# Kernel optimization log

Measured on AMD Instinct MI355X. Metric: run time of the kernel, lower is better.

Reference implementation:

```python
import jax, jax.numpy as jnp
import numpy as np

D_MODEL, D_K, D_V, H = 512, 64, 64, 8
B, NQ, NK = 2, 4096, 4096


def setup_inputs() -> dict:
    key = jax.random.key(0)
    ks = jax.random.split(key, 11)
    def xavier(k, shape):
        fan_in, fan_out = shape[1], shape[0]
        lim = jnp.sqrt(6.0 / (fan_in + fan_out))
        return jax.random.uniform(k, shape, jnp.float32, -lim, lim)
    return {
        "queries": jax.random.normal(ks[0], (B, NQ, D_MODEL), jnp.float32),
        "keys": jax.random.normal(ks[1], (B, NK, D_MODEL), jnp.float32),
        "values": jax.random.normal(ks[2], (B, NK, D_MODEL), jnp.float32),
        "Wq": xavier(ks[3], (H * D_K, D_MODEL)),
        "bq": jnp.zeros((H * D_K,), jnp.float32),
        "Wk": xavier(ks[4], (H * D_K, D_MODEL)),
        "bk": jnp.zeros((H * D_K,), jnp.float32),
        "Wv": xavier(ks[5], (H * D_V, D_MODEL)),
        "bv": jnp.zeros((H * D_V,), jnp.float32),
        "Wo": xavier(ks[6], (D_MODEL, H * D_V)),
        "bo": jnp.zeros((D_MODEL,), jnp.float32),
    }


def reference(queries, keys, values, Wq, bq, Wk, bk, Wv, bv, Wo, bo):
    b_s, nq, _ = queries.shape
    nk = keys.shape[1]
    # QKV projections (torch Linear: x @ W.T + b)
    q = (queries @ Wq.T + bq).reshape(b_s, nq, H, D_K).transpose(0, 2, 1, 3)  # b h nq dk
    k = (keys @ Wk.T + bk).reshape(b_s, nk, H, D_K).transpose(0, 2, 1, 3)     # b h nk dk
    v = (values @ Wv.T + bv).reshape(b_s, nk, H, D_V).transpose(0, 2, 1, 3)   # b h nk dv
    att = jnp.einsum("bhqd,bhkd->bhqk", q, k) / jnp.sqrt(jnp.float32(D_K))
    att = jax.nn.softmax(att, axis=-1)
    # dropout is identity in eval mode
    out = jnp.einsum("bhqk,bhkd->bhqd", att, v)
    out = out.transpose(0, 2, 1, 3).reshape(b_s, nq, H * D_V)
    return out @ Wo.T + bo
```

## Files before the change

### kernel.cpp

```cpp
#include <hip/hip_runtime.h>
#include <hip/hip_bf16.h>


typedef __attribute__((ext_vector_type(8))) short bf16x8;
typedef __attribute__((ext_vector_type(4))) float f32x4;
typedef __attribute__((ext_vector_type(16))) float f32x16;
typedef __attribute__((ext_vector_type(2))) int int2v;

#define SEQ  4096
#define DM   512
#define FPAD 72
#define VPAD 136
#define QSCALE 0.18033688011112042f
#define FSHIFT 16.0f

__device__ inline float fast_exp2(float x) {
#if __has_builtin(__builtin_amdgcn_exp2f)
    return __builtin_amdgcn_exp2f(x);
#else
    return __expf(x * 0.69314718056f);
#endif
}

__device__ inline unsigned pk2(float x, float y) {
#if __has_builtin(__builtin_amdgcn_cvt_pk_bf16_f32)
    typedef __attribute__((ext_vector_type(2))) __bf16 bf16x2_t;
    bf16x2_t h = __builtin_amdgcn_cvt_pk_bf16_f32(x, y);
    return *(unsigned*)&h;
#else
    unsigned ux = __float_as_uint(x);
    unsigned uy = __float_as_uint(y);
    ux += 0x7fff + ((ux >> 16) & 1);
    uy += 0x7fff + ((uy >> 16) & 1);
    return (ux >> 16) | (uy & 0xffff0000u);
#endif
}

__device__ inline int2v swap_half(unsigned a, unsigned b, int h) {
#if __has_builtin(__builtin_amdgcn_permlane32_swap)
    (void)h;
    return __builtin_amdgcn_permlane32_swap((int)a, (int)b, false, false);
#else
    unsigned ax = (unsigned)__shfl_xor((int)a, 32);
    unsigned bx = (unsigned)__shfl_xor((int)b, 32);
    int2v r;
    r.x = h ? (int)bx : (int)a;
    r.y = h ? (int)b  : (int)ax;
    return r;
#endif
}

__global__ __launch_bounds__(256) void cvt_w(
    const float* __restrict__ w0, const float* __restrict__ w1,
    const float* __restrict__ w2, const float* __restrict__ w3,
    __hip_bfloat16* __restrict__ o0, __hip_bfloat16* __restrict__ o1,
    __hip_bfloat16* __restrict__ o2, __hip_bfloat16* __restrict__ o3)
{
    const float* w = (blockIdx.y == 0) ? w0 : (blockIdx.y == 1) ? w1
                   : (blockIdx.y == 2) ? w2 : w3;
    __hip_bfloat16* o = (blockIdx.y == 0) ? o0 : (blockIdx.y == 1) ? o1
                      : (blockIdx.y == 2) ? o2 : o3;
    const int i = (blockIdx.x * 256 + threadIdx.x) * 4;
    float4 v = *(const float4*)&w[i];
    uint2 p;
    p.x = pk2(v.x, v.y);
    p.y = pk2(v.z, v.w);
    *(uint2*)&((unsigned short*)o)[i] = p;
}

__global__ __launch_bounds__(256) void qkv_proj(
    const float* __restrict__ Xq, const float* __restrict__ Xk, const float* __restrict__ Xv,
    const __hip_bfloat16* __restrict__ Wq16, const __hip_bfloat16* __restrict__ Wk16,
    const __hip_bfloat16* __restrict__ Wv16,
    const float* __restrict__ bq, const float* __restrict__ bk, const float* __restrict__ bv,
    __hip_bfloat16* __restrict__ Oq, __hip_bfloat16* __restrict__ Ok,
    __hip_bfloat16* __restrict__ Ovt)
{
    const int z = blockIdx.z;
    const float* A          = (z == 0) ? Xq : (z == 1) ? Xk : Xv;
    const __hip_bfloat16* W = (z == 0) ? Wq16 : (z == 1) ? Wk16 : Wv16;
    const float* bias       = (z == 0) ? bq : (z == 1) ? bk : bv;

    __shared__ __align__(16) short As[64 * 32];
    __shared__ __align__(16) short Ws2[128 * 32];

    const int bm   = blockIdx.x * 64;
    const int bn   = blockIdx.y * 128;
    const int tid  = threadIdx.x;
    const int wave = tid >> 6;
    const int lane = tid & 63;
    const int quad = lane >> 4;
    const int l16  = lane & 15;

    const int srow = tid >> 2;
    const int scol = (tid & 3) * 8;

    f32x4 acc[8] = {};

    float4 a0 = *(const float4*)&A[(size_t)(bm + srow) * DM + scol];
    float4 a1 = *(const float4*)&A[(size_t)(bm + srow) * DM + scol + 4];
    bf16x8 w0 = *(const bf16x8*)&W[(size_t)(bn + srow) * DM + scol];
    bf16x8 w1 = *(const bf16x8*)&W[(size_t)(bn + srow + 64) * DM + scol];

    for (int k0 = 0; k0 < DM; k0 += 32) {
        uint4 pa = {pk2(a0.x, a0.y), pk2(a0.z, a0.w), pk2(a1.x, a1.y), pk2(a1.z, a1.w)};

        __syncthreads();
        *(uint4*)&As[srow * 32 + scol] = pa;
        *(bf16x8*)&Ws2[srow * 32 + scol] = w0;
        *(bf16x8*)&Ws2[(srow + 64) * 32 + scol] = w1;
        __syncthreads();

        if (k0 + 32 < DM) {
            a0 = *(const float4*)&A[(size_t)(bm + srow) * DM + k0 + 32 + scol];
            a1 = *(const float4*)&A[(size_t)(bm + srow) * DM + k0 + 32 + scol + 4];
            w0 = *(const bf16x8*)&W[(size_t)(bn + srow) * DM + k0 + 32 + scol];
            w1 = *(const bf16x8*)&W[(size_t)(bn + srow + 64) * DM + k0 + 32 + scol];
        }

        bf16x8 a = *(bf16x8*)&As[(wave * 16 + l16) * 32 + quad * 8];
#pragma unroll
        for (int nt = 0; nt < 8; nt++) {
            bf16x8 b = *(bf16x8*)&Ws2[(nt * 16 + l16) * 32 + quad * 8];
            acc[nt] = __builtin_amdgcn_mfma_f32_16x16x32_bf16(a, b, acc[nt], 0, 0, 0);
        }
    }

    if (z == 2) {
        const int row0 = bm + wave * 16 + quad * 4;
        const int b    = row0 >> 12;
        const int seq0 = row0 & 4095;
        unsigned short* Vt = (unsigned short*)Ovt;
#pragma unroll
        for (int nt = 0; nt < 8; nt++) {
            const int col = bn + nt * 16 + l16;
            const float bv_ = bias[col];
            uint2 pk;
            pk.x = pk2(acc[nt][0] + bv_, acc[nt][1] + bv_);
            pk.y = pk2(acc[nt][2] + bv_, acc[nt][3] + bv_);
            *(uint2*)&Vt[((size_t)(b * 512 + col)) * 4096 + seq0] = pk;
        }
    } else {
        unsigned short* C = (unsigned short*)((z == 0) ? Oq : Ok);
        const float scale = (z == 0) ? QSCALE : 1.0f;
        const size_t row0 = bm + wave * 16 + quad * 4;
#pragma unroll
        for (int nt = 0; nt < 8; nt++) {
            const int col = bn + nt * 16 + l16;
            const float bv_ = bias[col];
            unsigned u01 = pk2((acc[nt][0] + bv_) * scale, (acc[nt][1] + bv_) * scale);
            unsigned u23 = pk2((acc[nt][2] + bv_) * scale, (acc[nt][3] + bv_) * scale);
            C[(row0 + 0) * DM + col] = (unsigned short)(u01 & 0xffff);
            C[(row0 + 1) * DM + col] = (unsigned short)(u01 >> 16);
            C[(row0 + 2) * DM + col] = (unsigned short)(u23 & 0xffff);
            C[(row0 + 3) * DM + col] = (unsigned short)(u23 >> 16);
        }
    }
}

__global__ __launch_bounds__(256, 4) void flash_attn(
    const __hip_bfloat16* __restrict__ Q,
    const __hip_bfloat16* __restrict__ K,
    const __hip_bfloat16* __restrict__ Vt,
    __hip_bfloat16* __restrict__ O)
{
    __shared__ __align__(16) short Ks[128 * FPAD];
    __shared__ __align__(16) short Vs[64 * VPAD];

    const int q0  = blockIdx.x * 128;
    const int bh  = blockIdx.y;
    const int tid = threadIdx.x;
    const int wave = tid >> 6;
    const int lane = tid & 63;
    const int L = lane & 31;
    const int h = lane >> 5;

    const __hip_bfloat16* Qb = Q + (size_t)(bh >> 3) * SEQ * DM + (bh & 7) * 64;
    const __hip_bfloat16* Kb = K + (size_t)(bh >> 3) * SEQ * DM + (bh & 7) * 64;
    const __hip_bfloat16* Vb = Vt + (size_t)bh * 64 * SEQ;
    __hip_bfloat16*       Ob = O + (size_t)(bh >> 3) * SEQ * DM + (bh & 7) * 64;

    const int kr = tid >> 3;
    const int kc = (tid & 7) * 8;
    const int vr = tid >> 4;
    const int vc = (tid & 15) * 8;

    const int qrow = q0 + wave * 32 + L;
    bf16x8 bq[4];
#pragma unroll
    for (int db = 0; db < 4; db++)
        bq[db] = *(const bf16x8*)&Qb[(size_t)qrow * DM + db * 16 + h * 8];

    const __hip_bfloat16* kg = Kb + (size_t)kr * DM + kc;
    const __hip_bfloat16* vg = Vb + (size_t)vr * SEQ + vc;

    bf16x8 kp[4], vp[4];
#pragma unroll
    for (int i = 0; i < 4; i++) {
        kp[i] = *(const bf16x8*)(kg + (size_t)i * 32 * DM);
        vp[i] = *(const bf16x8*)(vg + (size_t)i * 16 * SEQ);
    }

    const short* ksb = &Ks[L * FPAD + h * 8];
    const short* vsb = &Vs[L * VPAD + h * 8];

    f32x16 oacc[2] = {};
    float lsum = 0.0f;

    for (int kv0 = 0; kv0 < SEQ; kv0 += 128) {
        __syncthreads();
#pragma unroll
        for (int i = 0; i < 4; i++) {
            *(bf16x8*)&Ks[(kr + i * 32) * FPAD + kc] = kp[i];
            *(bf16x8*)&Vs[(vr + i * 16) * VPAD + vc] = vp[i];
        }
        __syncthreads();

        kg += (size_t)128 * DM;
        vg += 128;
        if (kv0 + 128 < SEQ) {
#pragma unroll
            for (int i = 0; i < 4; i++) {
                kp[i] = *(const bf16x8*)(kg + (size_t)i * 32 * DM);
                vp[i] = *(const bf16x8*)(vg + (size_t)i * 16 * SEQ);
            }
        }

#pragma unroll
        for (int kb = 0; kb < 4; kb++) {
            f32x16 s = {};
            __builtin_amdgcn_s_setprio(1);
#pragma unroll
            for (int db = 0; db < 4; db++) {
                bf16x8 ak = *(const bf16x8*)&ksb[(kb * 32) * FPAD + db * 16];
                s = __builtin_amdgcn_mfma_f32_32x32x16_bf16(ak, bq[db], s, 0, 0, 0);
            }
            __builtin_amdgcn_s_setprio(0);

#pragma unroll
            for (int r = 0; r < 16; r++) s[r] = fast_exp2(s[r] - FSHIFT);

            unsigned pk_[8];
#pragma unroll
            for (int j = 0; j < 8; j++) pk_[j] = pk2(s[2 * j], s[2 * j + 1]);

#pragma unroll
            for (int j = 0; j < 8; j++)
                lsum += __uint_as_float(pk_[j] << 16)
                      + __uint_as_float(pk_[j] & 0xffff0000u);

            int2v w0 = swap_half(pk_[0], pk_[2], h);
            int2v w1 = swap_half(pk_[1], pk_[3], h);
            int2v w2 = swap_half(pk_[4], pk_[6], h);
            int2v w3 = swap_half(pk_[5], pk_[7], h);
            uint4 f0u = {(unsigned)w0.x, (unsigned)w1.x, (unsigned)w0.y, (unsigned)w1.y};
            uint4 f1u = {(unsigned)w2.x, (unsigned)w3.x, (unsigned)w2.y, (unsigned)w3.y};
            bf16x8 fg0 = *(bf16x8*)&f0u;
            bf16x8 fg1 = *(bf16x8*)&f1u;

            __builtin_amdgcn_s_setprio(1);
#pragma unroll
            for (int dvb = 0; dvb < 2; dvb++) {
                bf16x8 av0 = *(const bf16x8*)&vsb[(dvb * 32) * VPAD + kb * 32];
                bf16x8 av1 = *(const bf16x8*)&vsb[(dvb * 32) * VPAD + kb * 32 + 16];
                oacc[dvb] = __builtin_amdgcn_mfma_f32_32x32x16_bf16(av0, fg0, oacc[dvb], 0, 0, 0);
                oacc[dvb] = __builtin_amdgcn_mfma_f32_32x32x16_bf16(av1, fg1, oacc[dvb], 0, 0, 0);
            }
            __builtin_amdgcn_s_setprio(0);
        }
    }

    const float tot = lsum + __shfl_xor(lsum, 32);
    const float inv = 1.0f / tot;

    unsigned short* Op = (unsigned short*)Ob;
#pragma unroll
    for (int dvb = 0; dvb < 2; dvb++)
#pragma unroll
        for (int b = 0; b < 4; b++) {
            uint2 ov;
            ov.x = pk2(oacc[dvb][4 * b + 0] * inv, oacc[dvb][4 * b + 1] * inv);
            ov.y = pk2(oacc[dvb][4 * b + 2] * inv, oacc[dvb][4 * b + 3] * inv);
            *(uint2*)&Op[(size_t)qrow * DM + dvb * 32 + b * 8 + h * 4] = ov;
        }
}

__global__ __launch_bounds__(256) void out_proj(
    const __hip_bfloat16* __restrict__ A,
    const __hip_bfloat16* __restrict__ W,
    const float* __restrict__ bias,
    float* __restrict__ C)
{
    __shared__ __align__(16) short As[64 * 32];
    __shared__ __align__(16) short Ws2[128 * 32];

    const int bm   = blockIdx.x * 64;
    const int bn   = blockIdx.y * 128;
    const int tid  = threadIdx.x;
    const int wave = tid >> 6;
    const int lane = tid & 63;
    const int quad = lane >> 4;
    const int l16  = lane & 15;

    const int srow = tid >> 2;
    const int scol = (tid & 3) * 8;

    f32x4 acc[8] = {};

    bf16x8 ap = *(const bf16x8*)&A[(size_t)(bm + srow) * DM + scol];
    bf16x8 w0 = *(const bf16x8*)&W[(size_t)(bn + srow) * DM + scol];
    bf16x8 w1 = *(const bf16x8*)&W[(size_t)(bn + srow + 64) * DM + scol];

    for (int k0 = 0; k0 < DM; k0 += 32) {
        __syncthreads();
        *(bf16x8*)&As[srow * 32 + scol] = ap;
        *(bf16x8*)&Ws2[srow * 32 + scol] = w0;
        *(bf16x8*)&Ws2[(srow + 64) * 32 + scol] = w1;
        __syncthreads();

        if (k0 + 32 < DM) {
            ap = *(const bf16x8*)&A[(size_t)(bm + srow) * DM + k0 + 32 + scol];
            w0 = *(const bf16x8*)&W[(size_t)(bn + srow) * DM + k0 + 32 + scol];
            w1 = *(const bf16x8*)&W[(size_t)(bn + srow + 64) * DM + k0 + 32 + scol];
        }

        bf16x8 a = *(bf16x8*)&As[(wave * 16 + l16) * 32 + quad * 8];
#pragma unroll
        for (int nt = 0; nt < 8; nt++) {
            bf16x8 b = *(bf16x8*)&Ws2[(nt * 16 + l16) * 32 + quad * 8];
            acc[nt] = __builtin_amdgcn_mfma_f32_16x16x32_bf16(a, b, acc[nt], 0, 0, 0);
        }
    }

#pragma unroll
    for (int nt = 0; nt < 8; nt++) {
        const int col = bn + nt * 16 + l16;
        const float bv_ = bias[col];
#pragma unroll
        for (int r = 0; r < 4; r++) {
            const int row = bm + wave * 16 + quad * 4 + r;
            C[(size_t)row * DM + col] = acc[nt][r] + bv_;
        }
    }
}

extern "C" void kernel_launch(void* const* d_in, const int* in_sizes, int n_in,
                              void* d_out, int out_size, void* d_ws, size_t ws_size,
                              hipStream_t stream) {
    const float* queries = (const float*)d_in[0];
    const float* keys    = (const float*)d_in[1];
    const float* values  = (const float*)d_in[2];
    const float* Wq = (const float*)d_in[3];
    const float* bq = (const float*)d_in[4];
    const float* Wk = (const float*)d_in[5];
    const float* bk = (const float*)d_in[6];
    const float* Wv = (const float*)d_in[7];
    const float* bv = (const float*)d_in[8];
    const float* Wo = (const float*)d_in[9];
    const float* bo = (const float*)d_in[10];
    float* out = (float*)d_out;

    const size_t MS = (size_t)2 * SEQ * DM;
    const size_t WN = (size_t)DM * DM;
    __hip_bfloat16* q_ws  = (__hip_bfloat16*)d_ws;
    __hip_bfloat16* k_ws  = q_ws + MS;
    __hip_bfloat16* vt_ws = k_ws + MS;
    __hip_bfloat16* o_ws  = vt_ws + MS;
    __hip_bfloat16* wq16  = o_ws + MS;
    __hip_bfloat16* wk16  = wq16 + WN;
    __hip_bfloat16* wv16  = wk16 + WN;
    __hip_bfloat16* wo16  = wv16 + WN;

    dim3 blk(256);

    cvt_w<<<dim3(256, 4), blk, 0, stream>>>(Wq, Wk, Wv, Wo, wq16, wk16, wv16, wo16);

    qkv_proj<<<dim3(128, 4, 3), blk, 0, stream>>>(
        queries, keys, values, wq16, wk16, wv16, bq, bk, bv, q_ws, k_ws, vt_ws);

    flash_attn<<<dim3(32, 16), blk, 0, stream>>>(q_ws, k_ws, vt_ws, o_ws);

    out_proj<<<dim3(128, 4), blk, 0, stream>>>(o_ws, wo16, bo, out);
}
```

Before: 251.3 us.

## Split KV tiles across two wave groups in flash attention with LDS reduction

Doubles the flash attention block to 512 threads: four query-row groups times two KV groups, each KV group handling half of every 128-key tile. This gives more waves per query tile to hide latency and halves per-thread global loads. Partial outputs and row sums are combined through shared memory at the end. The softmax shift is folded into the MFMA accumulator init, and the row sum is taken from fp32 values instead of the bf16-rounded ones. The costs are an extra reduction, more register and LDS pressure per block, and possibly lower occupancy under the 512-thread launch bound.

```diff
diff --git a/kernel.cpp b/kernel.cpp
--- a/kernel.cpp
+++ b/kernel.cpp
@@ -158,7 +158,7 @@
     }
 }
 
-__global__ __launch_bounds__(256, 4) void flash_attn(
+__global__ __launch_bounds__(512, 4) void flash_attn(
     const __hip_bfloat16* __restrict__ Q,
     const __hip_bfloat16* __restrict__ K,
     const __hip_bfloat16* __restrict__ Vt,
@@ -174,6 +174,8 @@
     const int lane = tid & 63;
     const int L = lane & 31;
     const int h = lane >> 5;
+    const int qg  = wave & 3;
+    const int kvg = wave >> 2;
 
     const __hip_bfloat16* Qb = Q + (size_t)(bh >> 3) * SEQ * DM + (bh & 7) * 64;
     const __hip_bfloat16* Kb = K + (size_t)(bh >> 3) * SEQ * DM + (bh & 7) * 64;
@@ -185,7 +187,7 @@
     const int vr = tid >> 4;
     const int vc = (tid & 15) * 8;
 
-    const int qrow = q0 + wave * 32 + L;
+    const int qrow = q0 + qg * 32 + L;
     bf16x8 bq[4];
 #pragma unroll
     for (int db = 0; db < 4; db++)
@@ -194,41 +196,41 @@
     const __hip_bfloat16* kg = Kb + (size_t)kr * DM + kc;
     const __hip_bfloat16* vg = Vb + (size_t)vr * SEQ + vc;
 
-    bf16x8 kp[4], vp[4];
-#pragma unroll
-    for (int i = 0; i < 4; i++) {
-        kp[i] = *(const bf16x8*)(kg + (size_t)i * 32 * DM);
-        vp[i] = *(const bf16x8*)(vg + (size_t)i * 16 * SEQ);
-    }
+    bf16x8 kp[2], vp[2];
+    kp[0] = *(const bf16x8*)(kg);
+    kp[1] = *(const bf16x8*)(kg + (size_t)64 * DM);
+    vp[0] = *(const bf16x8*)(vg);
+    vp[1] = *(const bf16x8*)(vg + (size_t)32 * SEQ);
 
     const short* ksb = &Ks[L * FPAD + h * 8];
     const short* vsb = &Vs[L * VPAD + h * 8];
 
     f32x16 oacc[2] = {};
-    float lsum = 0.0f;
+    float l0 = 0.0f, l1 = 0.0f;
 
     for (int kv0 = 0; kv0 < SEQ; kv0 += 128) {
         __syncthreads();
-#pragma unroll
-        for (int i = 0; i < 4; i++) {
-            *(bf16x8*)&Ks[(kr + i * 32) * FPAD + kc] = kp[i];
-            *(bf16x8*)&Vs[(vr + i * 16) * VPAD + vc] = vp[i];
-        }
+        *(bf16x8*)&Ks[kr * FPAD + kc] = kp[0];
+        *(bf16x8*)&Ks[(kr + 64) * FPAD + kc] = kp[1];
+        *(bf16x8*)&Vs[vr * VPAD + vc] = vp[0];
+        *(bf16x8*)&Vs[(vr + 32) * VPAD + vc] = vp[1];
         __syncthreads();
 
         kg += (size_t)128 * DM;
         vg += 128;
         if (kv0 + 128 < SEQ) {
-#pragma unroll
-            for (int i = 0; i < 4; i++) {
-                kp[i] = *(const bf16x8*)(kg + (size_t)i * 32 * DM);
-                vp[i] = *(const bf16x8*)(vg + (size_t)i * 16 * SEQ);
-            }
-        }
-
-#pragma unroll
-        for (int kb = 0; kb < 4; kb++) {
-            f32x16 s = {};
+            kp[0] = *(const bf16x8*)(kg);
+            kp[1] = *(const bf16x8*)(kg + (size_t)64 * DM);
+            vp[0] = *(const bf16x8*)(vg);
+            vp[1] = *(const bf16x8*)(vg + (size_t)32 * SEQ);
+        }
+
+#pragma unroll
+        for (int kb2 = 0; kb2 < 2; kb2++) {
+            const int kb = kvg * 2 + kb2;
+            f32x16 s;
+#pragma unroll
+            for (int r = 0; r < 16; r++) s[r] = -FSHIFT;
             __builtin_amdgcn_s_setprio(1);
 #pragma unroll
             for (int db = 0; db < 4; db++) {
@@ -238,16 +240,14 @@
             __builtin_amdgcn_s_setprio(0);
 
 #pragma unroll
-            for (int r = 0; r < 16; r++) s[r] = fast_exp2(s[r] - FSHIFT);
+            for (int r = 0; r < 16; r++) s[r] = fast_exp2(s[r]);
+
+#pragma unroll
+            for (int r = 0; r < 16; r += 2) { l0 += s[r]; l1 += s[r + 1]; }
 
             unsigned pk_[8];
 #pragma unroll
             for (int j = 0; j < 8; j++) pk_[j] = pk2(s[2 * j], s[2 * j + 1]);
-
-#pragma unroll
-            for (int j = 0; j < 8; j++)
-                lsum += __uint_as_float(pk_[j] << 16)
-                      + __uint_as_float(pk_[j] & 0xffff0000u);
 
             int2v w0 = swap_half(pk_[0], pk_[2], h);
             int2v w1 = swap_half(pk_[1], pk_[3], h);
@@ -270,19 +270,39 @@
         }
     }
 
-    const float tot = lsum + __shfl_xor(lsum, 32);
-    const float inv = 1.0f / tot;
-
-    unsigned short* Op = (unsigned short*)Ob;
-#pragma unroll
-    for (int dvb = 0; dvb < 2; dvb++)
-#pragma unroll
-        for (int b = 0; b < 4; b++) {
-            uint2 ov;
-            ov.x = pk2(oacc[dvb][4 * b + 0] * inv, oacc[dvb][4 * b + 1] * inv);
-            ov.y = pk2(oacc[dvb][4 * b + 2] * inv, oacc[dvb][4 * b + 3] * inv);
-            *(uint2*)&Op[(size_t)qrow * DM + dvb * 32 + b * 8 + h * 4] = ov;
-        }
+    float lsum = l0 + l1;
+    float tot = lsum + __shfl_xor(lsum, 32);
+
+    __syncthreads();
+    float* area = (qg < 2) ? (float*)Ks : (float*)Vs;
+    float* slot = area + (qg & 1) * (64 * 33) + lane * 33;
+    if (kvg == 1) {
+#pragma unroll
+        for (int dvb = 0; dvb < 2; dvb++)
+#pragma unroll
+            for (int r = 0; r < 16; r++) slot[dvb * 16 + r] = oacc[dvb][r];
+        slot[32] = tot;
+    }
+    __syncthreads();
+    if (kvg == 0) {
+#pragma unroll
+        for (int dvb = 0; dvb < 2; dvb++)
+#pragma unroll
+            for (int r = 0; r < 16; r++) oacc[dvb][r] += slot[dvb * 16 + r];
+        tot += slot[32];
+
+        const float inv = 1.0f / tot;
+        unsigned short* Op = (unsigned short*)Ob;
+#pragma unroll
+        for (int dvb = 0; dvb < 2; dvb++)
+#pragma unroll
+            for (int b = 0; b < 4; b++) {
+                uint2 ov;
+                ov.x = pk2(oacc[dvb][4 * b + 0] * inv, oacc[dvb][4 * b + 1] * inv);
+                ov.y = pk2(oacc[dvb][4 * b + 2] * inv, oacc[dvb][4 * b + 3] * inv);
+                *(uint2*)&Op[(size_t)qrow * DM + dvb * 32 + b * 8 + h * 4] = ov;
+            }
+    }
 }
 
 __global__ __launch_bounds__(256) void out_proj(
@@ -378,7 +398,7 @@
     qkv_proj<<<dim3(128, 4, 3), blk, 0, stream>>>(
         queries, keys, values, wq16, wk16, wv16, bq, bk, bv, q_ws, k_ws, vt_ws);
 
-    flash_attn<<<dim3(32, 16), blk, 0, stream>>>(q_ws, k_ws, vt_ws, o_ws);
+    flash_attn<<<dim3(32, 16), dim3(512), 0, stream>>>(q_ws, k_ws, vt_ws, o_ws);
 
     out_proj<<<dim3(128, 4), blk, 0, stream>>>(o_ws, wo16, bo, out);
 }
```

Measured after the change: 236.2 us. 6.0% less time.
